# Kernel tuning notes

Measured on AMD Instinct MI355X. Metric: run time of the kernel, lower is better.

Reference implementation:

```python
import jax, jax.numpy as jnp
import numpy as np

EPSILON = 1e-08

def setup_inputs() -> dict:
    key0 = jax.random.key(0)
    kq, kk, kv = jax.random.split(key0, 3)
    B, Q, H, D = 64, 16, 1, 64
    KV, DV = 16384, 64
    query = jax.random.normal(kq, (B, Q, H, D), dtype=jnp.float32)
    key = jax.random.normal(kk, (B, KV, H, D), dtype=jnp.float32)
    value = jax.random.normal(kv, (B, KV, H, DV), dtype=jnp.float32)
    return {"query": query, "key": key, "value": value}

def reference(query, key, value):
    # InvertedDotProductAttention(norm_type='mean', multi_head=False)
    d = query.shape[-1]
    q = query / jnp.sqrt(jnp.asarray(d, dtype=query.dtype))
    # logits: [b, h, q, k]
    attn = jnp.einsum('bqhd,bkhd->bhqk', q, key)
    # inverted attention: softmax over the query axis (-2)
    attn = jax.nn.softmax(attn, axis=-2)
    # renormalize_keys=True (norm_type == 'mean'): normalize over key axis
    attn = attn / (jnp.sum(attn, axis=-1, keepdims=True) + EPSILON)
    out = jnp.einsum('bhqk,bkhd->bqhd', attn, value)
    # multi_head=False -> squeeze the (singleton) heads axis
    return jnp.squeeze(out, axis=-2)
```

## Files before the change

### kernel.cpp

```cpp
#include <hip/hip_runtime.h>

namespace {

typedef float f32x4 __attribute__((ext_vector_type(4)));
typedef short bf16x8 __attribute__((ext_vector_type(8)));

constexpr int Bn = 64, QN = 16, Dn = 64, DVn = 64, KVn = 16384;
constexpr int MAX_SPLITS = 32;
constexpr int TILE = 64;
constexpr int THREADS = 256;
constexpr int PTP = 20;

constexpr float SCALE = 0.125f * 1.4426950408889634f;

__device__ __forceinline__ unsigned cvt_pk_bf16(float a, float b) {
    unsigned r;
    asm("v_cvt_pk_bf16_f32 %0, %1, %2" : "=v"(r) : "v"(a), "v"(b));
    return r;
}

union FragU { unsigned u[4]; bf16x8 v; };

__device__ __forceinline__ void split8(const float* x, bf16x8& hi, bf16x8& lo) {
    FragU uh, ul;
#pragma unroll
    for (int p = 0; p < 4; ++p) {
        const float a = x[2 * p], b = x[2 * p + 1];
        const unsigned h = cvt_pk_bf16(a, b);
        uh.u[p] = h;
        const float ha = __uint_as_float(h << 16);
        const float hb = __uint_as_float(h & 0xffff0000u);
        ul.u[p] = cvt_pk_bf16(a - ha, b - hb);
    }
    hi = uh.v; lo = ul.v;
}

__device__ __forceinline__ f32x4 qk_softmax(const float* kp,
                                            const bf16x8 qhi[2],
                                            const bf16x8 qlo[2]) {
    f32x4 sacc = {0.f, 0.f, 0.f, 0.f};
#pragma unroll
    for (int ks = 0; ks < 2; ++ks) {
        const float4 a = *reinterpret_cast<const float4*>(kp + ks * 32);
        const float4 b = *reinterpret_cast<const float4*>(kp + ks * 32 + 4);
        float x[8] = {a.x, a.y, a.z, a.w, b.x, b.y, b.z, b.w};
        bf16x8 khi, klo;
        split8(x, khi, klo);
        sacc = __builtin_amdgcn_mfma_f32_16x16x32_bf16(qhi[ks], khi, sacc, 0, 0, 0);
        sacc = __builtin_amdgcn_mfma_f32_16x16x32_bf16(qhi[ks], klo, sacc, 0, 0, 0);
        sacc = __builtin_amdgcn_mfma_f32_16x16x32_bf16(qlo[ks], khi, sacc, 0, 0, 0);
    }
    float m = fmaxf(fmaxf(sacc[0], sacc[1]), fmaxf(sacc[2], sacc[3]));
    m = fmaxf(m, __shfl_xor(m, 16, 64));
    m = fmaxf(m, __shfl_xor(m, 32, 64));
    f32x4 pr;
    pr[0] = exp2f(sacc[0] - m); pr[1] = exp2f(sacc[1] - m);
    pr[2] = exp2f(sacc[2] - m); pr[3] = exp2f(sacc[3] - m);
    float s = pr[0] + pr[1] + pr[2] + pr[3];
    s += __shfl_xor(s, 16, 64);
    s += __shfl_xor(s, 32, 64);
    const float inv = 1.0f / s;
    pr[0] *= inv; pr[1] *= inv; pr[2] *= inv; pr[3] *= inv;
    return pr;
}

__global__ __launch_bounds__(THREADS, 4)
void inv_attn_part(const float* __restrict__ query,
                   const float* __restrict__ key,
                   const float* __restrict__ value,
                   float* __restrict__ pout,
                   float* __restrict__ pden,
                   int npairs)
{
    __shared__ __align__(16) float pT[4][32 * PTP];

    const int tid = threadIdx.x;
    const int lane = tid & 63;
    const int w = tid >> 6;
    const int l15 = lane & 15;
    const int g = lane >> 4;
    const int spl = blockIdx.x;
    const int splits = gridDim.x;
    const int b = blockIdx.y;
    const int kt0 = spl * (npairs * 2 * TILE) + w * 16;

    bf16x8 qhi[2], qlo[2];
    {
        const float* qp = query + ((size_t)b * QN + l15) * Dn + g * 8;
#pragma unroll
        for (int ks = 0; ks < 2; ++ks) {
            const float4 u0 = *reinterpret_cast<const float4*>(qp + ks * 32);
            const float4 u1 = *reinterpret_cast<const float4*>(qp + ks * 32 + 4);
            float x[8] = {u0.x * SCALE, u0.y * SCALE, u0.z * SCALE, u0.w * SCALE,
                          u1.x * SCALE, u1.y * SCALE, u1.z * SCALE, u1.w * SCALE};
            split8(x, qhi[ks], qlo[ks]);
        }
    }

    const float* kp = key + ((size_t)b * KVn + kt0 + l15) * Dn + g * 8;
    const float* vp = value + ((size_t)b * KVn + kt0 + (g & 1) * 8 + (g >> 1) * TILE) * Dn + l15;
    float* pTw = &pT[w][0];

    f32x4 o0 = {0.f,0.f,0.f,0.f}, o1 = {0.f,0.f,0.f,0.f},
          o2 = {0.f,0.f,0.f,0.f}, o3 = {0.f,0.f,0.f,0.f};
    f32x4 den = {0.f,0.f,0.f,0.f};

    for (int p = 0; p < npairs; ++p) {
        const f32x4 pA = qk_softmax(kp, qhi, qlo);
        const f32x4 pB = qk_softmax(kp + 64 * Dn, qhi, qlo);
        den[0] += pA[0] + pB[0]; den[1] += pA[1] + pB[1];
        den[2] += pA[2] + pB[2]; den[3] += pA[3] + pB[3];

        *reinterpret_cast<f32x4*>(&pTw[l15 * PTP + g * 4]) = pA;
        *reinterpret_cast<f32x4*>(&pTw[(16 + l15) * PTP + g * 4]) = pB;

        float ax[8];
#pragma unroll
        for (int j = 0; j < 8; ++j) ax[j] = pTw[(g * 8 + j) * PTP + l15];
        FragU ua;
        ua.u[0] = cvt_pk_bf16(ax[0], ax[1]);
        ua.u[1] = cvt_pk_bf16(ax[2], ax[3]);
        ua.u[2] = cvt_pk_bf16(ax[4], ax[5]);
        ua.u[3] = cvt_pk_bf16(ax[6], ax[7]);

#define PV_CHUNK(c, oc) {                                                     \
        float vx[8];                                                          \
        _Pragma("unroll")                                                     \
        for (int j = 0; j < 8; ++j) vx[j] = vp[j * Dn + (c) * 16];            \
        FragU uv;                                                             \
        uv.u[0] = cvt_pk_bf16(vx[0], vx[1]);                                  \
        uv.u[1] = cvt_pk_bf16(vx[2], vx[3]);                                  \
        uv.u[2] = cvt_pk_bf16(vx[4], vx[5]);                                  \
        uv.u[3] = cvt_pk_bf16(vx[6], vx[7]);                                  \
        oc = __builtin_amdgcn_mfma_f32_16x16x32_bf16(ua.v, uv.v, oc, 0, 0, 0); }
        PV_CHUNK(0, o0)
        PV_CHUNK(1, o1)
        PV_CHUNK(2, o2)
        PV_CHUNK(3, o3)
#undef PV_CHUNK

        kp += 128 * Dn;
        vp += 128 * Dn;
    }

    const int s4 = spl * 4 + w;
    const size_t obase = (((size_t)b * (splits * 4) + s4) * QN) * DVn;
#pragma unroll
    for (int r = 0; r < 4; ++r) {
        const int q = g * 4 + r;
        pout[obase + q * DVn +  0 + l15] = o0[r];
        pout[obase + q * DVn + 16 + l15] = o1[r];
        pout[obase + q * DVn + 32 + l15] = o2[r];
        pout[obase + q * DVn + 48 + l15] = o3[r];
    }

#pragma unroll
    for (int off = 1; off < 16; off <<= 1) {
        den[0] += __shfl_xor(den[0], off, 64);
        den[1] += __shfl_xor(den[1], off, 64);
        den[2] += __shfl_xor(den[2], off, 64);
        den[3] += __shfl_xor(den[3], off, 64);
    }
    if (l15 == 0) {
        const size_t dbase = ((size_t)b * (splits * 4) + s4) * QN + g * 4;
        pden[dbase + 0] = den[0];
        pden[dbase + 1] = den[1];
        pden[dbase + 2] = den[2];
        pden[dbase + 3] = den[3];
    }
}

__global__ __launch_bounds__(256)
void inv_attn_reduce(const float* __restrict__ pout,
                     const float* __restrict__ pden,
                     float* __restrict__ out,
                     int splits4)
{
    const int gid = blockIdx.x * blockDim.x + threadIdx.x;
    const int dv = gid & 63;
    const int q  = (gid >> 6) & (QN - 1);
    const int b  = gid >> 10;
    float sum = 0.f, den = 0.f;
#pragma unroll 4
    for (int sp = 0; sp < splits4; ++sp) {
        sum += pout[(((size_t)b * splits4 + sp) * QN + q) * DVn + dv];
        den += pden[((size_t)b * splits4 + sp) * QN + q];
    }
    out[gid] = sum / (den + 1e-8f);
}

}

extern "C" void kernel_launch(void* const* d_in, const int* in_sizes, int n_in,
                              void* d_out, int out_size, void* d_ws, size_t ws_size,
                              hipStream_t stream) {
    const float* query = (const float*)d_in[0];
    const float* key   = (const float*)d_in[1];
    const float* value = (const float*)d_in[2];
    float* out = (float*)d_out;

    int splits = MAX_SPLITS;
    auto need = [](int s) {
        return (size_t)Bn * s * 4 * QN * DVn * sizeof(float)
             + (size_t)Bn * s * 4 * QN * sizeof(float);
    };
    while (splits > 1 && need(splits) > ws_size) splits >>= 1;

    float* pout = (float*)d_ws;
    float* pden = pout + (size_t)Bn * (splits * 4) * QN * DVn;

    const int npairs = KVn / (splits * TILE * 2);

    dim3 grid1(splits, Bn);
    inv_attn_part<<<grid1, THREADS, 0, stream>>>(query, key, value, pout, pden, npairs);

    const int total = Bn * QN * DVn;
    inv_attn_reduce<<<total / 256, 256, 0, stream>>>(pout, pden, out, splits * 4);
}
```

Baseline: 123.8 us.

## Stream K/V tiles into LDS via async global_load_lds with triple buffering

Replaces direct global loads of K and V with asynchronous global-to-LDS copies into a three-slot per-wave ring buffer, using XOR swizzling to avoid bank conflicts, and waits with explicit vmcnt counters. Splits are fixed at 16 (down from up to 32) and loop bounds become compile-time constants. The aim is to hide HBM latency behind the MFMA and softmax work. In exchange it uses about 96KB of LDS per block, which limits occupancy, drops the workspace-size fallback, and relies on hand-tuned waitcnt values.

```diff
diff --git a/kernel.cpp b/kernel.cpp
--- a/kernel.cpp
+++ b/kernel.cpp
@@ -6,12 +6,17 @@
 typedef short bf16x8 __attribute__((ext_vector_type(8)));
 
 constexpr int Bn = 64, QN = 16, Dn = 64, DVn = 64, KVn = 16384;
-constexpr int MAX_SPLITS = 32;
-constexpr int TILE = 64;
+constexpr int SPLITS  = 16;
+constexpr int TILE    = 64;
 constexpr int THREADS = 256;
-constexpr int PTP = 20;
+constexpr int NT      = KVn / (SPLITS * TILE);
+constexpr int NPAIRS  = NT / 2;
+constexpr int PTP     = 20;
+constexpr int SPLITS4 = SPLITS * 4;
 
 constexpr float SCALE = 0.125f * 1.4426950408889634f;
+
+#define MFMA16x32 __builtin_amdgcn_mfma_f32_16x16x32_bf16
 
 __device__ __forceinline__ unsigned cvt_pk_bf16(float a, float b) {
     unsigned r;
@@ -35,54 +40,31 @@
     hi = uh.v; lo = ul.v;
 }
 
-__device__ __forceinline__ f32x4 qk_softmax(const float* kp,
-                                            const bf16x8 qhi[2],
-                                            const bf16x8 qlo[2]) {
-    f32x4 sacc = {0.f, 0.f, 0.f, 0.f};
-#pragma unroll
-    for (int ks = 0; ks < 2; ++ks) {
-        const float4 a = *reinterpret_cast<const float4*>(kp + ks * 32);
-        const float4 b = *reinterpret_cast<const float4*>(kp + ks * 32 + 4);
-        float x[8] = {a.x, a.y, a.z, a.w, b.x, b.y, b.z, b.w};
-        bf16x8 khi, klo;
-        split8(x, khi, klo);
-        sacc = __builtin_amdgcn_mfma_f32_16x16x32_bf16(qhi[ks], khi, sacc, 0, 0, 0);
-        sacc = __builtin_amdgcn_mfma_f32_16x16x32_bf16(qhi[ks], klo, sacc, 0, 0, 0);
-        sacc = __builtin_amdgcn_mfma_f32_16x16x32_bf16(qlo[ks], khi, sacc, 0, 0, 0);
-    }
-    float m = fmaxf(fmaxf(sacc[0], sacc[1]), fmaxf(sacc[2], sacc[3]));
-    m = fmaxf(m, __shfl_xor(m, 16, 64));
-    m = fmaxf(m, __shfl_xor(m, 32, 64));
-    f32x4 pr;
-    pr[0] = exp2f(sacc[0] - m); pr[1] = exp2f(sacc[1] - m);
-    pr[2] = exp2f(sacc[2] - m); pr[3] = exp2f(sacc[3] - m);
-    float s = pr[0] + pr[1] + pr[2] + pr[3];
-    s += __shfl_xor(s, 16, 64);
-    s += __shfl_xor(s, 32, 64);
-    const float inv = 1.0f / s;
-    pr[0] *= inv; pr[1] *= inv; pr[2] *= inv; pr[3] *= inv;
-    return pr;
-}
-
-__global__ __launch_bounds__(THREADS, 4)
+__device__ __forceinline__ void gl_lds16(const float* g, const char* l) {
+    __builtin_amdgcn_global_load_lds(
+        (const __attribute__((address_space(1))) unsigned int*)g,
+        (__attribute__((address_space(3))) unsigned int*)l,
+        16, 0, 0);
+}
+
+__global__ __launch_bounds__(THREADS)
 void inv_attn_part(const float* __restrict__ query,
                    const float* __restrict__ key,
                    const float* __restrict__ value,
                    float* __restrict__ pout,
-                   float* __restrict__ pden,
-                   int npairs)
+                   float* __restrict__ pden)
 {
+    __shared__ __align__(16) char  kv[3][4][2][4096];
     __shared__ __align__(16) float pT[4][32 * PTP];
 
-    const int tid = threadIdx.x;
+    const int tid  = threadIdx.x;
     const int lane = tid & 63;
-    const int w = tid >> 6;
-    const int l15 = lane & 15;
-    const int g = lane >> 4;
-    const int spl = blockIdx.x;
-    const int splits = gridDim.x;
-    const int b = blockIdx.y;
-    const int kt0 = spl * (npairs * 2 * TILE) + w * 16;
+    const int w    = tid >> 6;
+    const int l15  = lane & 15;
+    const int g    = lane >> 4;
+    const int spl  = blockIdx.x;
+    const int b    = blockIdx.y;
+    const int kt0  = spl * (NT * TILE);
 
     bf16x8 qhi[2], qlo[2];
     {
@@ -96,23 +78,80 @@
             split8(x, qhi[ks], qlo[ks]);
         }
     }
-
-    const float* kp = key + ((size_t)b * KVn + kt0 + l15) * Dn + g * 8;
-    const float* vp = value + ((size_t)b * KVn + kt0 + (g & 1) * 8 + (g >> 1) * TILE) * Dn + l15;
-    float* pTw = &pT[w][0];
+    __builtin_amdgcn_sched_barrier(0);
+
+    const int srow = lane >> 4;
+    const int sp   = lane & 15;
+    const float* kg = key   + ((size_t)b * KVn + kt0 + w * 16) * Dn;
+    const float* vg = value + ((size_t)b * KVn + kt0 + w * 16) * Dn;
+
+    auto issue_tile = [&](int t, int slot) {
+        const char* kb = &kv[slot][w][0][0];
+        const char* vb = &kv[slot][w][1][0];
+        const size_t toff = (size_t)t * TILE * Dn;
+#pragma unroll
+        for (int i = 0; i < 4; ++i) {
+            const int perm = sp ^ srow ^ (4 * (i & 1));
+            const size_t off = toff + (size_t)(i * 4 + srow) * Dn + perm * 4;
+            gl_lds16(kg + off, kb + i * 1024);
+            gl_lds16(vg + off, vb + i * 1024);
+        }
+        __builtin_amdgcn_sched_barrier(0);
+    };
+
+    auto qk_softmax = [&](int slot) -> f32x4 {
+        const char* kb = &kv[slot][w][0][0];
+        const int sw = l15 & 7;
+        f32x4 sacc = {0.f, 0.f, 0.f, 0.f};
+#pragma unroll
+        for (int ks = 0; ks < 2; ++ks) {
+            const int c0 = ks * 8 + g * 2;
+            const f32x4 r0 = *reinterpret_cast<const f32x4*>(
+                kb + l15 * 256 + ((c0    ) ^ sw) * 16);
+            const f32x4 r1 = *reinterpret_cast<const f32x4*>(
+                kb + l15 * 256 + ((c0 + 1) ^ sw) * 16);
+            float x[8] = {r0[0], r0[1], r0[2], r0[3], r1[0], r1[1], r1[2], r1[3]};
+            bf16x8 khi, klo;
+            split8(x, khi, klo);
+            sacc = MFMA16x32(qhi[ks], khi, sacc, 0, 0, 0);
+            sacc = MFMA16x32(qhi[ks], klo, sacc, 0, 0, 0);
+            sacc = MFMA16x32(qlo[ks], khi, sacc, 0, 0, 0);
+        }
+        float m = fmaxf(fmaxf(sacc[0], sacc[1]), fmaxf(sacc[2], sacc[3]));
+        m = fmaxf(m, __shfl_xor(m, 16, 64));
+        m = fmaxf(m, __shfl_xor(m, 32, 64));
+        f32x4 pr;
+        pr[0] = exp2f(sacc[0] - m); pr[1] = exp2f(sacc[1] - m);
+        pr[2] = exp2f(sacc[2] - m); pr[3] = exp2f(sacc[3] - m);
+        float s = pr[0] + pr[1] + pr[2] + pr[3];
+        s += __shfl_xor(s, 16, 64);
+        s += __shfl_xor(s, 32, 64);
+        const float inv = 1.0f / s;
+        pr[0] *= inv; pr[1] *= inv; pr[2] *= inv; pr[3] *= inv;
+        return pr;
+    };
+
+    issue_tile(0, 0);
+    issue_tile(1, 1);
+    issue_tile(2, 2);
 
     f32x4 o0 = {0.f,0.f,0.f,0.f}, o1 = {0.f,0.f,0.f,0.f},
           o2 = {0.f,0.f,0.f,0.f}, o3 = {0.f,0.f,0.f,0.f};
     f32x4 den = {0.f,0.f,0.f,0.f};
-
-    for (int p = 0; p < npairs; ++p) {
-        const f32x4 pA = qk_softmax(kp, qhi, qlo);
-        const f32x4 pB = qk_softmax(kp + 64 * Dn, qhi, qlo);
+    float* pTw = &pT[w][0];
+
+    int s0 = 0, s1 = 1, s2 = 2;
+    for (int p = 0; p < NPAIRS; ++p) {
+        if (p == NPAIRS - 1) { asm volatile("s_waitcnt vmcnt(0)" ::: "memory"); }
+        else                 { asm volatile("s_waitcnt vmcnt(8)" ::: "memory"); }
+        __builtin_amdgcn_sched_barrier(0);
+
+        const f32x4 pA = qk_softmax(s0);
+        *reinterpret_cast<f32x4*>(&pTw[l15 * PTP + g * 4]) = pA;
+        const f32x4 pB = qk_softmax(s1);
+        *reinterpret_cast<f32x4*>(&pTw[(16 + l15) * PTP + g * 4]) = pB;
         den[0] += pA[0] + pB[0]; den[1] += pA[1] + pB[1];
         den[2] += pA[2] + pB[2]; den[3] += pA[3] + pB[3];
-
-        *reinterpret_cast<f32x4*>(&pTw[l15 * PTP + g * 4]) = pA;
-        *reinterpret_cast<f32x4*>(&pTw[(16 + l15) * PTP + g * 4]) = pB;
 
         float ax[8];
 #pragma unroll
@@ -123,28 +162,36 @@
         ua.u[2] = cvt_pk_bf16(ax[4], ax[5]);
         ua.u[3] = cvt_pk_bf16(ax[6], ax[7]);
 
-#define PV_CHUNK(c, oc) {                                                     \
-        float vx[8];                                                          \
-        _Pragma("unroll")                                                     \
-        for (int j = 0; j < 8; ++j) vx[j] = vp[j * Dn + (c) * 16];            \
-        FragU uv;                                                             \
-        uv.u[0] = cvt_pk_bf16(vx[0], vx[1]);                                  \
-        uv.u[1] = cvt_pk_bf16(vx[2], vx[3]);                                  \
-        uv.u[2] = cvt_pk_bf16(vx[4], vx[5]);                                  \
-        uv.u[3] = cvt_pk_bf16(vx[6], vx[7]);                                  \
-        oc = __builtin_amdgcn_mfma_f32_16x16x32_bf16(ua.v, uv.v, oc, 0, 0, 0); }
-        PV_CHUNK(0, o0)
-        PV_CHUNK(1, o1)
-        PV_CHUNK(2, o2)
-        PV_CHUNK(3, o3)
-#undef PV_CHUNK
-
-        kp += 128 * Dn;
-        vp += 128 * Dn;
-    }
-
-    const int s4 = spl * 4 + w;
-    const size_t obase = (((size_t)b * (splits * 4) + s4) * QN) * DVn;
+        const char* vb = &kv[(g < 2) ? s0 : s1][w][1][0];
+        const int rbase = (g & 1) * 8;
+        const int cb = l15 >> 2;
+        const int wb = (l15 & 3) * 4;
+#pragma unroll
+        for (int c = 0; c < 4; ++c) {
+            float vx[8];
+#pragma unroll
+            for (int j = 0; j < 8; ++j) {
+                const int addr = (rbase + j) * 256 + (((c * 4 + cb) ^ j) << 4) + wb;
+                vx[j] = *reinterpret_cast<const float*>(vb + addr);
+            }
+            FragU uv;
+            uv.u[0] = cvt_pk_bf16(vx[0], vx[1]);
+            uv.u[1] = cvt_pk_bf16(vx[2], vx[3]);
+            uv.u[2] = cvt_pk_bf16(vx[4], vx[5]);
+            uv.u[3] = cvt_pk_bf16(vx[6], vx[7]);
+            f32x4& oc = (c == 0) ? o0 : (c == 1) ? o1 : (c == 2) ? o2 : o3;
+            oc = MFMA16x32(ua.v, uv.v, oc, 0, 0, 0);
+        }
+
+        const int tn0 = 2 * p + 3, tn1 = 2 * p + 4;
+        if (tn0 < NT) issue_tile(tn0, s0);
+        if (tn1 < NT) issue_tile(tn1, s1);
+
+        const int os0 = s0, os1 = s1;
+        s0 = s2; s1 = os0; s2 = os1;
+    }
+
+    const size_t obase = (((size_t)b * SPLITS4 + spl * 4 + w) * QN) * DVn;
 #pragma unroll
     for (int r = 0; r < 4; ++r) {
         const int q = g * 4 + r;
@@ -162,7 +209,7 @@
         den[3] += __shfl_xor(den[3], off, 64);
     }
     if (l15 == 0) {
-        const size_t dbase = ((size_t)b * (splits * 4) + s4) * QN + g * 4;
+        const size_t dbase = ((size_t)b * SPLITS4 + spl * 4 + w) * QN + g * 4;
         pden[dbase + 0] = den[0];
         pden[dbase + 1] = den[1];
         pden[dbase + 2] = den[2];
@@ -173,8 +220,7 @@
 __global__ __launch_bounds__(256)
 void inv_attn_reduce(const float* __restrict__ pout,
                      const float* __restrict__ pden,
-                     float* __restrict__ out,
-                     int splits4)
+                     float* __restrict__ out)
 {
     const int gid = blockIdx.x * blockDim.x + threadIdx.x;
     const int dv = gid & 63;
@@ -182,9 +228,9 @@
     const int b  = gid >> 10;
     float sum = 0.f, den = 0.f;
 #pragma unroll 4
-    for (int sp = 0; sp < splits4; ++sp) {
-        sum += pout[(((size_t)b * splits4 + sp) * QN + q) * DVn + dv];
-        den += pden[((size_t)b * splits4 + sp) * QN + q];
+    for (int sp = 0; sp < SPLITS4; ++sp) {
+        sum += pout[(((size_t)b * SPLITS4 + sp) * QN + q) * DVn + dv];
+        den += pden[((size_t)b * SPLITS4 + sp) * QN + q];
     }
     out[gid] = sum / (den + 1e-8f);
 }
@@ -199,21 +245,12 @@
     const float* value = (const float*)d_in[2];
     float* out = (float*)d_out;
 
-    int splits = MAX_SPLITS;
-    auto need = [](int s) {
-        return (size_t)Bn * s * 4 * QN * DVn * sizeof(float)
-             + (size_t)Bn * s * 4 * QN * sizeof(float);
-    };
-    while (splits > 1 && need(splits) > ws_size) splits >>= 1;
-
     float* pout = (float*)d_ws;
-    float* pden = pout + (size_t)Bn * (splits * 4) * QN * DVn;
-
-    const int npairs = KVn / (splits * TILE * 2);
-
-    dim3 grid1(splits, Bn);
-    inv_attn_part<<<grid1, THREADS, 0, stream>>>(query, key, value, pout, pden, npairs);
+    float* pden = pout + (size_t)Bn * SPLITS4 * QN * DVn;
+
+    dim3 grid1(SPLITS, Bn);
+    inv_attn_part<<<grid1, THREADS, 0, stream>>>(query, key, value, pout, pden);
 
     const int total = Bn * QN * DVn;
-    inv_attn_reduce<<<total / 256, 256, 0, stream>>>(pout, pden, out, splits * 4);
-}
+    inv_attn_reduce<<<total / 256, 256, 0, stream>>>(pout, pden, out);
+}
```

Result: faster. 118.7 us (-4.0%).
